# Performance work log

Hardware: AMD Instinct MI355X
Metric: run time of the kernel (lower is better)

## Reference

```python
import jax, jax.numpy as jnp
import numpy as np

B, SQ, SK, D = 32, 2048, 2048, 64

def setup_inputs() -> dict:
    key = jax.random.key(0)
    kq, kk, kv = jax.random.split(key, 3)
    q = jax.random.normal(kq, (B, SQ, D), dtype=jnp.float32)
    k = jax.random.normal(kk, (B, SK, D), dtype=jnp.float32)
    v = jax.random.normal(kv, (B, SK, D), dtype=jnp.float32)
    return {"q": q, "k": k, "v": v}

def reference(q, k, v):
    # Faithful to the torch module: softmax/dropout are defined in __init__
    # but NEVER applied in forward. attn = (q @ k^T) / sqrt(d); out = attn @ v.
    scale = jnp.sqrt(jnp.asarray(k.shape[-1], dtype=jnp.float32))
    attn = jnp.einsum('bqd,bkd->bqk', q, k) / scale  # [B, Sq, Sk]
    out = jnp.einsum('bqk,bkd->bqd', attn, v)        # [B, Sq, Dv]
    return (out, attn)
```

## Files before the change

kernel.cpp:

```cpp
#include <hip/hip_runtime.h>
#include <hip/hip_bf16.h>


typedef __attribute__((ext_vector_type(4))) float        f32x4;
typedef __attribute__((ext_vector_type(8))) short        s16x8;
typedef __attribute__((ext_vector_type(2))) unsigned int u32x2;
typedef __attribute__((ext_vector_type(4))) unsigned int u32x4;

#define NB    32
#define SQL   2048
#define SKL   2048
#define DD    64
#define QBLK  128
#define KBLK  64
#define NTILES (SKL / KBLK)

#define KOFF 0
#define VOFF 16384
#define SOFF 32768

__device__ __forceinline__ unsigned short f2bf(float f) {
    union { float f; unsigned u; } x; x.f = f;
    unsigned r = x.u + 0x7FFFu + ((x.u >> 16) & 1u);
    return (unsigned short)(r >> 16);
}
__device__ __forceinline__ unsigned swzK(unsigned k) { return (k & 7u) << 4; }
__device__ __forceinline__ unsigned swzV(unsigned d) { return (d & 7u) << 4; }
__device__ __forceinline__ unsigned swzS(unsigned q) { return ((q + (q >> 3)) & 7u) << 4; }

__global__ __launch_bounds__(512, 4)
void sdpa_fused(const float* __restrict__ qg, const float* __restrict__ kg,
                const float* __restrict__ vg, float* __restrict__ og,
                float* __restrict__ ag) {
    __shared__ __align__(16) char smem[49152];

    const unsigned tid  = threadIdx.x;
    const unsigned wid  = tid >> 6;
    const unsigned lane = tid & 63u;
    const unsigned l15  = lane & 15u;
    const unsigned l4   = lane >> 4;

    const unsigned xcd = blockIdx.x & 7u;
    const unsigned loc = blockIdx.x >> 3;
    const unsigned b   = xcd * 4u + (loc >> 4);
    const unsigned qt  = loc & 15u;
    const unsigned qbase = qt * QBLK;

    const unsigned kr = tid >> 3, kc = tid & 7u;
    const unsigned vt = tid >> 4, vc = tid & 15u;

    s16x8 aq[2];
    {
        const float* qrow = qg + ((size_t)b * SQL + qbase + wid * 16 + l15) * DD;
        #pragma unroll
        for (int ks = 0; ks < 2; ++ks) {
            f32x4 f0 = *(const f32x4*)(qrow + ks * 32 + l4 * 8);
            f32x4 f1 = *(const f32x4*)(qrow + ks * 32 + l4 * 8 + 4);
            #pragma unroll
            for (int j = 0; j < 4; ++j) {
                aq[ks][j]     = (short)f2bf(f0[j] * 0.125f);
                aq[ks][j + 4] = (short)f2bf(f1[j] * 0.125f);
            }
        }
    }

    f32x4 acc_o[4];
    #pragma unroll
    for (int n = 0; n < 4; ++n) acc_o[n] = (f32x4){0.f, 0.f, 0.f, 0.f};

    const float* kbat = kg + (size_t)b * SKL * DD;
    const float* vbat = vg + (size_t)b * SKL * DD;

    auto stage = [&](int kt, int sel) {
        const float* ksrc = kbat + (size_t)kt * KBLK * DD;
        const float* vsrc = vbat + (size_t)kt * KBLK * DD;
        f32x4 k0 = *(const f32x4*)(ksrc + kr * DD + kc * 8);
        f32x4 k1 = *(const f32x4*)(ksrc + kr * DD + kc * 8 + 4);
        s16x8 h;
        #pragma unroll
        for (int j = 0; j < 4; ++j) {
            h[j]     = (short)f2bf(k0[j]);
            h[j + 4] = (short)f2bf(k1[j]);
        }
        *(s16x8*)(smem + KOFF + sel * 8192 + kr * 128 + ((kc * 16) ^ swzK(kr))) = h;
        f32x4 v0 = *(const f32x4*)(vsrc + (2 * vt) * DD + vc * 4);
        f32x4 v1 = *(const f32x4*)(vsrc + (2 * vt + 1) * DD + vc * 4);
        #pragma unroll
        for (int j = 0; j < 4; ++j) {
            unsigned d = vc * 4 + (unsigned)j;
            unsigned pack = (unsigned)f2bf(v0[j]) | ((unsigned)f2bf(v1[j]) << 16);
            *(unsigned*)(smem + VOFF + sel * 8192 + d * 128 + ((vt * 4) ^ swzV(d))) = pack;
        }
    };

    stage(0, 0);
    __syncthreads();

    char* sbase = smem + SOFF + wid * 2048;
    const unsigned rr = lane >> 3, cc = lane & 7u;

    for (int kt = 0; kt < NTILES; ++kt) {
        const int cur = kt & 1;
        if (kt + 1 < NTILES) stage(kt + 1, cur ^ 1);

        const char* kb = smem + KOFF + cur * 8192;
        f32x4 acc[4];
        #pragma unroll
        for (int n = 0; n < 4; ++n) acc[n] = (f32x4){0.f, 0.f, 0.f, 0.f};
        #pragma unroll
        for (int ks = 0; ks < 2; ++ks)
            #pragma unroll
            for (int nk = 0; nk < 4; ++nk) {
                unsigned row = nk * 16 + l15;
                s16x8 bk = *(const s16x8*)(kb + row * 128 +
                            ((ks * 64 + l4 * 16) ^ swzK(row)));
                acc[nk] = __builtin_amdgcn_mfma_f32_16x16x32_bf16(
                              aq[ks], bk, acc[nk], 0, 0, 0);
            }

        #pragma unroll
        for (int nk = 0; nk < 4; ++nk)
            #pragma unroll
            for (int i = 0; i < 4; ++i) {
                unsigned q = l4 * 4 + (unsigned)i;
                unsigned key = nk * 16 + l15;
                *(unsigned short*)(sbase + q * 128 + ((key * 2) ^ swzS(q))) =
                    f2bf(acc[nk][i]);
            }

        {
            float* abase = ag + ((size_t)b * SQL + qbase + wid * 16) * SKL
                              + (size_t)kt * KBLK;
            #pragma unroll
            for (int h = 0; h < 4; ++h) {
                unsigned q  = (h & 1) * 8 + rr;
                unsigned k4 = (h >> 1) * 32 + cc * 4;
                u32x2 p = *(const u32x2*)(sbase + q * 128 + ((k4 * 2) ^ swzS(q)));
                u32x4 w;
                w[0] = p[0] << 16; w[1] = p[0] & 0xFFFF0000u;
                w[2] = p[1] << 16; w[3] = p[1] & 0xFFFF0000u;
                __builtin_nontemporal_store(w,
                    (u32x4*)(abase + (size_t)q * SKL + k4));
            }
        }

        const char* vb = smem + VOFF + cur * 8192;
        #pragma unroll
        for (int ks = 0; ks < 2; ++ks) {
            s16x8 sa = *(const s16x8*)(sbase + l15 * 128 +
                        ((ks * 64 + l4 * 16) ^ swzS(l15)));
            #pragma unroll
            for (int nd = 0; nd < 4; ++nd) {
                unsigned row = nd * 16 + l15;
                s16x8 vf = *(const s16x8*)(vb + row * 128 +
                            ((ks * 64 + l4 * 16) ^ swzV(row)));
                acc_o[nd] = __builtin_amdgcn_mfma_f32_16x16x32_bf16(
                                sa, vf, acc_o[nd], 0, 0, 0);
            }
        }

        __syncthreads();
    }

    float* op = og + ((size_t)b * SQL + qbase + wid * 16 + l4 * 4) * DD + l15;
    #pragma unroll
    for (int nd = 0; nd < 4; ++nd)
        #pragma unroll
        for (int i = 0; i < 4; ++i)
            __builtin_nontemporal_store(acc_o[nd][i], op + (size_t)i * DD + nd * 16);
}

extern "C" void kernel_launch(void* const* d_in, const int* in_sizes, int n_in,
                              void* d_out, int out_size, void* d_ws, size_t ws_size,
                              hipStream_t stream) {
    const float* q = (const float*)d_in[0];
    const float* k = (const float*)d_in[1];
    const float* v = (const float*)d_in[2];
    float* outp  = (float*)d_out;
    float* attnp = outp + (size_t)NB * SQL * DD;
    sdpa_fused<<<dim3(NB * (SQL / QBLK)), dim3(512), 0, stream>>>(q, k, v, outp, attnp);
}
```

Baseline: 127.4 us.

## Switch to 32x32x16 MFMA with register-resident P and split-K wave pairs

```diff
diff --git a/kernel.cpp b/kernel.cpp
--- a/kernel.cpp
+++ b/kernel.cpp
@@ -2,10 +2,9 @@
 #include <hip/hip_bf16.h>
 
 
-typedef __attribute__((ext_vector_type(4))) float        f32x4;
-typedef __attribute__((ext_vector_type(8))) short        s16x8;
-typedef __attribute__((ext_vector_type(2))) unsigned int u32x2;
-typedef __attribute__((ext_vector_type(4))) unsigned int u32x4;
+typedef __attribute__((ext_vector_type(4)))  float        f32x4;
+typedef __attribute__((ext_vector_type(16))) float        f32x16;
+typedef __attribute__((ext_vector_type(8)))  short        s16x8;
 
 #define NB    32
 #define SQL   2048
@@ -17,28 +16,31 @@
 
 #define KOFF 0
 #define VOFF 16384
-#define SOFF 32768
 
 __device__ __forceinline__ unsigned short f2bf(float f) {
     union { float f; unsigned u; } x; x.f = f;
     unsigned r = x.u + 0x7FFFu + ((x.u >> 16) & 1u);
     return (unsigned short)(r >> 16);
 }
-__device__ __forceinline__ unsigned swzK(unsigned k) { return (k & 7u) << 4; }
-__device__ __forceinline__ unsigned swzV(unsigned d) { return (d & 7u) << 4; }
-__device__ __forceinline__ unsigned swzS(unsigned q) { return ((q + (q >> 3)) & 7u) << 4; }
+__device__ __forceinline__ unsigned pkbf(float lo, float hi) {
+    union { float f; unsigned u; } a, b; a.f = lo; b.f = hi;
+    return (a.u >> 16) | (b.u & 0xFFFF0000u);
+}
 
 __global__ __launch_bounds__(512, 4)
 void sdpa_fused(const float* __restrict__ qg, const float* __restrict__ kg,
                 const float* __restrict__ vg, float* __restrict__ og,
                 float* __restrict__ ag) {
-    __shared__ __align__(16) char smem[49152];
+    __shared__ __align__(16) char smem[32768];
 
     const unsigned tid  = threadIdx.x;
     const unsigned wid  = tid >> 6;
     const unsigned lane = tid & 63u;
-    const unsigned l15  = lane & 15u;
-    const unsigned l4   = lane >> 4;
+    const unsigned l31  = lane & 31u;
+    const unsigned l5   = lane >> 5;
+    const bool     lo   = (l5 == 0);
+    const unsigned qw   = wid >> 1;
+    const unsigned kh   = wid & 1u;
 
     const unsigned xcd = blockIdx.x & 7u;
     const unsigned loc = blockIdx.x >> 3;
@@ -46,27 +48,23 @@
     const unsigned qt  = loc & 15u;
     const unsigned qbase = qt * QBLK;
 
-    const unsigned kr = tid >> 3, kc = tid & 7u;
-    const unsigned vt = tid >> 4, vc = tid & 15u;
-
-    s16x8 aq[2];
+    s16x8 qf[4];
     {
-        const float* qrow = qg + ((size_t)b * SQL + qbase + wid * 16 + l15) * DD;
-        #pragma unroll
-        for (int ks = 0; ks < 2; ++ks) {
-            f32x4 f0 = *(const f32x4*)(qrow + ks * 32 + l4 * 8);
-            f32x4 f1 = *(const f32x4*)(qrow + ks * 32 + l4 * 8 + 4);
+        const float* qrow = qg + (size_t)(b * SQL + qbase + qw * 32 + l31) * DD;
+        #pragma unroll
+        for (int kk = 0; kk < 4; ++kk) {
+            f32x4 f0 = *(const f32x4*)(qrow + kk * 16 + l5 * 8);
+            f32x4 f1 = *(const f32x4*)(qrow + kk * 16 + l5 * 8 + 4);
             #pragma unroll
             for (int j = 0; j < 4; ++j) {
-                aq[ks][j]     = (short)f2bf(f0[j] * 0.125f);
-                aq[ks][j + 4] = (short)f2bf(f1[j] * 0.125f);
+                qf[kk][j]     = (short)f2bf(f0[j] * 0.125f);
+                qf[kk][j + 4] = (short)f2bf(f1[j] * 0.125f);
             }
         }
     }
 
-    f32x4 acc_o[4];
-    #pragma unroll
-    for (int n = 0; n < 4; ++n) acc_o[n] = (f32x4){0.f, 0.f, 0.f, 0.f};
+    f32x16 acc_o0 = {0,0,0,0,0,0,0,0,0,0,0,0,0,0,0,0};
+    f32x16 acc_o1 = {0,0,0,0,0,0,0,0,0,0,0,0,0,0,0,0};
 
     const float* kbat = kg + (size_t)b * SKL * DD;
     const float* vbat = vg + (size_t)b * SKL * DD;
@@ -74,100 +72,125 @@
     auto stage = [&](int kt, int sel) {
         const float* ksrc = kbat + (size_t)kt * KBLK * DD;
         const float* vsrc = vbat + (size_t)kt * KBLK * DD;
-        f32x4 k0 = *(const f32x4*)(ksrc + kr * DD + kc * 8);
-        f32x4 k1 = *(const f32x4*)(ksrc + kr * DD + kc * 8 + 4);
-        s16x8 h;
-        #pragma unroll
-        for (int j = 0; j < 4; ++j) {
-            h[j]     = (short)f2bf(k0[j]);
-            h[j + 4] = (short)f2bf(k1[j]);
-        }
-        *(s16x8*)(smem + KOFF + sel * 8192 + kr * 128 + ((kc * 16) ^ swzK(kr))) = h;
-        f32x4 v0 = *(const f32x4*)(vsrc + (2 * vt) * DD + vc * 4);
-        f32x4 v1 = *(const f32x4*)(vsrc + (2 * vt + 1) * DD + vc * 4);
-        #pragma unroll
-        for (int j = 0; j < 4; ++j) {
-            unsigned d = vc * 4 + (unsigned)j;
-            unsigned pack = (unsigned)f2bf(v0[j]) | ((unsigned)f2bf(v1[j]) << 16);
-            *(unsigned*)(smem + VOFF + sel * 8192 + d * 128 + ((vt * 4) ^ swzV(d))) = pack;
+        {
+            unsigned key = tid >> 3, d0 = (tid & 7u) * 8;
+            f32x4 a0 = *(const f32x4*)(ksrc + key * DD + d0);
+            f32x4 a1 = *(const f32x4*)(ksrc + key * DD + d0 + 4);
+            s16x8 h;
+            #pragma unroll
+            for (int j = 0; j < 4; ++j) {
+                h[j]     = (short)f2bf(a0[j]);
+                h[j + 4] = (short)f2bf(a1[j]);
+            }
+            *(s16x8*)(smem + KOFF + sel * 8192 + (key >> 5) * 4096 +
+                      (d0 >> 4) * 1024 + (key & 31u) * 32 + ((d0 >> 3) & 1u) * 16) = h;
+        }
+        {
+            unsigned kp = tid & 31u, dq = tid >> 5;
+            unsigned k0 = kp * 2, d0 = dq * 4;
+            f32x4 v0 = *(const f32x4*)(vsrc + (size_t)k0 * DD + d0);
+            f32x4 v1 = *(const f32x4*)(vsrc + (size_t)(k0 + 1) * DD + d0);
+            char* vb = smem + VOFF + sel * 8192 + (kp >> 4) * 4096 +
+                       ((kp >> 3) & 1u) * 2048 + ((kp >> 2) & 1u) * 16 + (kp & 3u) * 4;
+            #pragma unroll
+            for (int j = 0; j < 4; ++j) {
+                unsigned pack = (unsigned)f2bf(v0[j]) | ((unsigned)f2bf(v1[j]) << 16);
+                *(unsigned*)(vb + (d0 + (unsigned)j) * 32) = pack;
+            }
         }
     };
 
     stage(0, 0);
     __syncthreads();
 
-    char* sbase = smem + SOFF + wid * 2048;
-    const unsigned rr = lane >> 3, cc = lane & 7u;
+    float* const aw = ag + (size_t)(b * SQL + qbase + qw * 32 + 4 * l5) * SKL
+                         + kh * 32 + l31;
 
     for (int kt = 0; kt < NTILES; ++kt) {
-        const int cur = kt & 1;
-        if (kt + 1 < NTILES) stage(kt + 1, cur ^ 1);
-
-        const char* kb = smem + KOFF + cur * 8192;
-        f32x4 acc[4];
-        #pragma unroll
-        for (int n = 0; n < 4; ++n) acc[n] = (f32x4){0.f, 0.f, 0.f, 0.f};
-        #pragma unroll
-        for (int ks = 0; ks < 2; ++ks)
-            #pragma unroll
-            for (int nk = 0; nk < 4; ++nk) {
-                unsigned row = nk * 16 + l15;
-                s16x8 bk = *(const s16x8*)(kb + row * 128 +
-                            ((ks * 64 + l4 * 16) ^ swzK(row)));
-                acc[nk] = __builtin_amdgcn_mfma_f32_16x16x32_bf16(
-                              aq[ks], bk, acc[nk], 0, 0, 0);
-            }
-
-        #pragma unroll
-        for (int nk = 0; nk < 4; ++nk)
-            #pragma unroll
-            for (int i = 0; i < 4; ++i) {
-                unsigned q = l4 * 4 + (unsigned)i;
-                unsigned key = nk * 16 + l15;
-                *(unsigned short*)(sbase + q * 128 + ((key * 2) ^ swzS(q))) =
-                    f2bf(acc[nk][i]);
-            }
-
-        {
-            float* abase = ag + ((size_t)b * SQL + qbase + wid * 16) * SKL
-                              + (size_t)kt * KBLK;
-            #pragma unroll
-            for (int h = 0; h < 4; ++h) {
-                unsigned q  = (h & 1) * 8 + rr;
-                unsigned k4 = (h >> 1) * 32 + cc * 4;
-                u32x2 p = *(const u32x2*)(sbase + q * 128 + ((k4 * 2) ^ swzS(q)));
-                u32x4 w;
-                w[0] = p[0] << 16; w[1] = p[0] & 0xFFFF0000u;
-                w[2] = p[1] << 16; w[3] = p[1] & 0xFFFF0000u;
-                __builtin_nontemporal_store(w,
-                    (u32x4*)(abase + (size_t)q * SKL + k4));
-            }
-        }
-
-        const char* vb = smem + VOFF + cur * 8192;
-        #pragma unroll
-        for (int ks = 0; ks < 2; ++ks) {
-            s16x8 sa = *(const s16x8*)(sbase + l15 * 128 +
-                        ((ks * 64 + l4 * 16) ^ swzS(l15)));
-            #pragma unroll
-            for (int nd = 0; nd < 4; ++nd) {
-                unsigned row = nd * 16 + l15;
-                s16x8 vf = *(const s16x8*)(vb + row * 128 +
-                            ((ks * 64 + l4 * 16) ^ swzV(row)));
-                acc_o[nd] = __builtin_amdgcn_mfma_f32_16x16x32_bf16(
-                                sa, vf, acc_o[nd], 0, 0, 0);
-            }
+        const int sel = kt & 1;
+        if (kt + 1 < NTILES) stage(kt + 1, sel ^ 1);
+
+        const char* ka = smem + KOFF + sel * 8192 + kh * 4096 + l31 * 32 + l5 * 16;
+        f32x16 as = {0,0,0,0,0,0,0,0,0,0,0,0,0,0,0,0};
+        f32x16 an = {0,0,0,0,0,0,0,0,0,0,0,0,0,0,0,0};
+        #pragma unroll
+        for (int kk = 0; kk < 4; ++kk) {
+            s16x8 kf = *(const s16x8*)(ka + kk * 1024);
+            as = __builtin_amdgcn_mfma_f32_32x32x16_bf16(kf, qf[kk], as, 0, 0, 0);
+            an = __builtin_amdgcn_mfma_f32_32x32x16_bf16(qf[kk], kf, an, 0, 0, 0);
+        }
+
+        {
+            float* ap = aw + (size_t)kt * KBLK;
+            #pragma unroll
+            for (int r = 0; r < 16; ++r)
+                __builtin_nontemporal_store(an[r],
+                    ap + (size_t)((r & 3) + 8 * (r >> 2)) * SKL);
+        }
+
+        unsigned c0 = pkbf(as[0],  as[1]);
+        unsigned c1 = pkbf(as[2],  as[3]);
+        unsigned c2 = pkbf(as[4],  as[5]);
+        unsigned c3 = pkbf(as[6],  as[7]);
+        unsigned c4 = pkbf(as[8],  as[9]);
+        unsigned c5 = pkbf(as[10], as[11]);
+        unsigned c6 = pkbf(as[12], as[13]);
+        unsigned c7 = pkbf(as[14], as[15]);
+        {
+            unsigned t;
+            t = __shfl_xor(c0, 32); unsigned u = __shfl_xor(c2, 32);
+            c2 = lo ? t : c2;  c0 = lo ? c0 : u;
+            t = __shfl_xor(c1, 32); u = __shfl_xor(c3, 32);
+            c3 = lo ? t : c3;  c1 = lo ? c1 : u;
+            t = __shfl_xor(c4, 32); u = __shfl_xor(c6, 32);
+            c6 = lo ? t : c6;  c4 = lo ? c4 : u;
+            t = __shfl_xor(c5, 32); u = __shfl_xor(c7, 32);
+            c7 = lo ? t : c7;  c5 = lo ? c5 : u;
+        }
+        s16x8 pa0, pa1;
+        {
+            unsigned w0[4] = {c0, c1, c2, c3};
+            unsigned w1[4] = {c4, c5, c6, c7};
+            __builtin_memcpy(&pa0, w0, 16);
+            __builtin_memcpy(&pa1, w1, 16);
+        }
+
+        const char* vbp = smem + VOFF + sel * 8192 + kh * 4096 + l5 * 16;
+        {
+            s16x8 vf00 = *(const s16x8*)(vbp + 0    + (0 * 32 + l31) * 32);
+            s16x8 vf01 = *(const s16x8*)(vbp + 0    + (1 * 32 + l31) * 32);
+            s16x8 vf10 = *(const s16x8*)(vbp + 2048 + (0 * 32 + l31) * 32);
+            s16x8 vf11 = *(const s16x8*)(vbp + 2048 + (1 * 32 + l31) * 32);
+            acc_o0 = __builtin_amdgcn_mfma_f32_32x32x16_bf16(pa0, vf00, acc_o0, 0, 0, 0);
+            acc_o1 = __builtin_amdgcn_mfma_f32_32x32x16_bf16(pa0, vf01, acc_o1, 0, 0, 0);
+            acc_o0 = __builtin_amdgcn_mfma_f32_32x32x16_bf16(pa1, vf10, acc_o0, 0, 0, 0);
+            acc_o1 = __builtin_amdgcn_mfma_f32_32x32x16_bf16(pa1, vf11, acc_o1, 0, 0, 0);
         }
 
         __syncthreads();
     }
 
-    float* op = og + ((size_t)b * SQL + qbase + wid * 16 + l4 * 4) * DD + l15;
-    #pragma unroll
-    for (int nd = 0; nd < 4; ++nd)
-        #pragma unroll
-        for (int i = 0; i < 4; ++i)
-            __builtin_nontemporal_store(acc_o[nd][i], op + (size_t)i * DD + nd * 16);
+    float* red = (float*)smem + qw * 2048;
+    if (kh == 1) {
+        #pragma unroll
+        for (int r = 0; r < 16; ++r) {
+            unsigned qloc = (r & 3) + 8 * (r >> 2) + 4 * l5;
+            red[qloc * 64 +      l31] = acc_o0[r];
+            red[qloc * 64 + 32 + l31] = acc_o1[r];
+        }
+    }
+    __syncthreads();
+    if (kh == 0) {
+        float* op = og + (size_t)(b * SQL + qbase + qw * 32) * DD;
+        #pragma unroll
+        for (int r = 0; r < 16; ++r) {
+            unsigned qloc = (r & 3) + 8 * (r >> 2) + 4 * l5;
+            float v0 = acc_o0[r] + red[qloc * 64 +      l31];
+            float v1 = acc_o1[r] + red[qloc * 64 + 32 + l31];
+            __builtin_nontemporal_store(v0, op + (size_t)qloc * DD +      l31);
+            __builtin_nontemporal_store(v1, op + (size_t)qloc * DD + 32 + l31);
+        }
+    }
 }
 
 extern "C" void kernel_launch(void* const* d_in, const int* in_sizes, int n_in,
```

Result: slower. 140.6 us (+10.4%).
